# Optimization experiments

Hardware: AMD Instinct MI355X
Metric: run time of the kernel (lower is better)

Reference implementation:

```python
import jax, jax.numpy as jnp
import numpy as np

NEG_SLOPE_GAT = 0.2   # PyG GATConv default negative_slope
NEG_SLOPE = 0.01      # torch.nn.LeakyReLU default
NUM_AISLES = 20       # aisle_nrs drawn from [0,20); matches aisle_nrs.max()+1


def leaky(x, s):
    return jnp.where(x >= 0, x, s * x)


def gat_conv(x, src, dst, W, a_src, a_dst, b, n_nodes):
    """Single-head PyG GATConv (self-loops already appended to src/dst)."""
    h = x @ W                                        # [N, C]
    es = h @ a_src                                   # [N]
    ed = h @ a_dst                                   # [N]
    e = leaky(es[src] + ed[dst], NEG_SLOPE_GAT)      # [E] per-edge score
    m = jax.ops.segment_max(e, dst, num_segments=n_nodes)
    w = jnp.exp(e - m[dst])
    z = jax.ops.segment_sum(w, dst, num_segments=n_nodes)
    alpha = w / z[dst]                               # segment softmax over incoming edges
    out = jax.ops.segment_sum(h[src] * alpha[:, None], dst, num_segments=n_nodes)
    return out + b


def setup_inputs() -> dict:
    key = jax.random.key(0)
    ks = jax.random.split(key, 32)
    B, N, E = 16, 2048, 32768
    Fin, H, O, HA = 32, 128, 64, 256

    def glorot(k, shape):
        fan = shape[0] + shape[-1]
        return jax.random.uniform(k, shape, jnp.float32, -1.0, 1.0) * np.sqrt(6.0 / fan)

    inp = {
        "graph_nodes": jax.random.normal(ks[0], (B, N, Fin), jnp.float32),
        "aisle_nrs": jax.random.randint(ks[1], (B, N), 0, NUM_AISLES),
        "graph_edge_links": jax.random.randint(ks[2], (B, 2, E), 0, N),
        "mask": jax.random.randint(ks[3], (B, N), 0, 2),
        "picks_left": jax.random.randint(ks[4], (B,), 0, 100),
        # GAT layer 1: Fin -> H
        "W1": glorot(ks[5], (Fin, H)), "as1": glorot(ks[6], (H,)), "ad1": glorot(ks[7], (H,)), "b1": jnp.zeros((H,), jnp.float32),
        # GAT layer 2: H -> H
        "W2": glorot(ks[8], (H, H)), "as2": glorot(ks[9], (H,)), "ad2": glorot(ks[10], (H,)), "b2": jnp.zeros((H,), jnp.float32),
        # GAT layer 3: H -> O
        "W3": glorot(ks[11], (H, O)), "as3": glorot(ks[12], (O,)), "ad3": glorot(ks[13], (O,)), "b3": jnp.zeros((O,), jnp.float32),
        # post-embedding MLP head
        "lw1": glorot(ks[14], (2 * O, HA)), "lb1": jnp.zeros((HA,), jnp.float32),
        "lw2": glorot(ks[15], (HA, O)), "lb2": jnp.zeros((O,), jnp.float32),
        "lw3": glorot(ks[16], (O, 1)), "lb3": jnp.zeros((1,), jnp.float32),
    }
    return inp


def reference(graph_nodes, aisle_nrs, graph_edge_links, mask, picks_left,
              W1, as1, ad1, b1, W2, as2, ad2, b2, W3, as3, ad3, b3,
              lw1, lb1, lw2, lb2, lw3, lb3):
    B, N, Fin = graph_nodes.shape
    NT = B * N
    x = graph_nodes.reshape(NT, Fin)

    # batch the graphs: offset per-graph edge indices, append self-loops
    off = (jnp.arange(B) * N)[:, None]
    src = (graph_edge_links[:, 0, :] + off).reshape(-1)
    dst = (graph_edge_links[:, 1, :] + off).reshape(-1)
    loops = jnp.arange(NT)
    src = jnp.concatenate([src, loops])
    dst = jnp.concatenate([dst, loops])

    x = gat_conv(x, src, dst, W1, as1, ad1, b1, NT)
    x = gat_conv(x, src, dst, W2, as2, ad2, b2, NT)
    x = gat_conv(x, src, dst, W3, as3, ad3, b3, NT)

    # scatter-mean aisle embedding
    batch_idx = jnp.repeat(jnp.arange(B), N)
    aid = aisle_nrs.reshape(-1) + batch_idx * NUM_AISLES   # [NT]
    S = B * NUM_AISLES
    ssum = jax.ops.segment_sum(x, aid, num_segments=S)
    cnt = jax.ops.segment_sum(jnp.ones((NT,), x.dtype), aid, num_segments=S)
    emb = ssum / jnp.maximum(cnt, 1.0)[:, None]

    x = jnp.concatenate([x, emb[aid]], axis=1)             # [NT, 2*O]
    x = leaky(x @ lw1 + lb1, NEG_SLOPE)
    x = leaky(x @ lw2 + lb2, NEG_SLOPE)
    x = (x @ lw3 + lb3).reshape(B, N)

    logits = jnp.where(mask != 0, x, -jnp.inf)
    return jax.nn.softmax(logits, axis=1)
```

## Files before the change

kernel.cpp:

```cpp
#include <hip/hip_runtime.h>
#include <hip/hip_bf16.h>
#include <math.h>

#define BATCH 16
#define NNODE 2048
#define EPG   32768
#define NT    (BATCH * NNODE)
#define ET    (BATCH * EPG + NT)
#define NUM_AISLES 20
#define SEG   (BATCH * NUM_AISLES)
#define NEG_GAT 0.2f
#define NEG_MLP 0.01f
#define ACHUNK 8
#define CAP 64

typedef __attribute__((ext_vector_type(8))) short s16x8;
typedef __attribute__((ext_vector_type(4))) float f32x4;

__device__ __forceinline__ void split_bf16(float v, unsigned short& hi, unsigned short& lo) {
    unsigned int u = __float_as_uint(v);
    unsigned int r = u + 0x7FFFu + ((u >> 16) & 1u);
    hi = (unsigned short)(r >> 16);
    float fh = __uint_as_float(((unsigned int)hi) << 16);
    float rem = v - fh;
    unsigned int u2 = __float_as_uint(rem);
    unsigned int r2 = u2 + 0x7FFFu + ((u2 >> 16) & 1u);
    lo = (unsigned short)(r2 >> 16);
}

#define WT_W1  0
#define WT_W2  4096
#define WT_W3  20480
#define WT_LW1 28672
#define WT_LW2 61440
#define WT_TOT 77824

__global__ __launch_bounds__(256) void wsplit_kernel(const float* __restrict__ W1,
                                                     const float* __restrict__ W2,
                                                     const float* __restrict__ W3,
                                                     const float* __restrict__ lw1,
                                                     const float* __restrict__ lw2,
                                                     unsigned short* __restrict__ wt_hi,
                                                     unsigned short* __restrict__ wt_lo) {
    int idx = blockIdx.x * 256 + threadIdx.x;
    if (idx >= WT_TOT) return;
    const float* src;
    int base, K, N;
    if (idx < WT_W2)      { src = W1;  base = WT_W1;  K = 32;  N = 128; }
    else if (idx < WT_W3) { src = W2;  base = WT_W2;  K = 128; N = 128; }
    else if (idx < WT_LW1){ src = W3;  base = WT_W3;  K = 128; N = 64;  }
    else if (idx < WT_LW2){ src = lw1; base = WT_LW1; K = 128; N = 256; }
    else                  { src = lw2; base = WT_LW2; K = 256; N = 64;  }
    int local = idx - base;
    int k = local / N;
    int n = local - k * N;
    unsigned short hi, lo;
    split_bf16(src[(size_t)k * N + n], hi, lo);
    wt_hi[base + (size_t)n * K + k] = hi;
    wt_lo[base + (size_t)n * K + k] = lo;
}

__global__ __launch_bounds__(256) void edge_scatter(const int* __restrict__ links,
                                                    int* __restrict__ cnt,
                                                    int* __restrict__ col_bkt) {
    int b = blockIdx.x;
    int s, d;
    if (b < 2048) {
        int xcd = b & 7, idx = b >> 3;
        int g = xcd * 2 + (idx >> 7);
        int chunk = idx & 127;
        int i = chunk * 256 + threadIdx.x;
        const int* pb = links + (size_t)g * 2 * EPG;
        s = pb[i] + (g << 11);
        d = pb[EPG + i] + (g << 11);
    } else {
        int b2 = b - 2048;
        int xcd = b2 & 7, idx = b2 >> 3;
        int g = xcd * 2 + (idx >> 3);
        int chunk = idx & 7;
        s = d = g * NNODE + chunk * 256 + threadIdx.x;
    }
    int pos = atomicAdd(&cnt[d], 1);
    if (pos < CAP) col_bkt[d * CAP + pos] = s;
}

template <int K, int NOUT, int COLS, bool LEAKY, bool ATTN, bool FINAL, bool CONCAT>
__global__ __launch_bounds__(256) void gemm_mfma(const float* __restrict__ A,
                                                 const unsigned short* __restrict__ wt_hi,
                                                 const unsigned short* __restrict__ wt_lo,
                                                 const float* __restrict__ bias,
                                                 float* __restrict__ out,
                                                 const float* __restrict__ a_src,
                                                 const float* __restrict__ a_dst,
                                                 float* __restrict__ es,
                                                 float* __restrict__ ed,
                                                 const float* __restrict__ emb,
                                                 const int* __restrict__ aisle,
                                                 const float* __restrict__ lw3,
                                                 const float* __restrict__ lb3,
                                                 const int* __restrict__ mask,
                                                 float* __restrict__ logits) {
    constexpr int C = COLS / 16;

    const int tid = threadIdx.x;
    const int wave = tid >> 6, lane = tid & 63;
    const int quad = lane >> 4, l15 = lane & 15;
    const int row0 = blockIdx.x * 64;
    const int c0 = blockIdx.y * COLS;
    const int m = row0 + wave * 16 + l15;

    f32x4 acc[C];
#pragma unroll
    for (int c = 0; c < C; ++c)
#pragma unroll
        for (int v = 0; v < 4; ++v) acc[c][v] = 0.f;

    union SU { s16x8 v; unsigned short u[8]; };

    for (int kc = 0; kc < K; kc += 32) {
        const int off = kc + quad * 8;
        const float* srcp;
        if constexpr (CONCAT) {
            if (off < 64) {
                srcp = A + (size_t)m * 64 + off;
            } else {
                int g = m >> 11;
                srcp = emb + ((size_t)(g * NUM_AISLES + aisle[m])) * 64 + (off - 64);
            }
        } else {
            srcp = A + (size_t)m * K + off;
        }
        float4 v0 = ((const float4*)srcp)[0];
        float4 v1 = ((const float4*)srcp)[1];
        float a8[8] = {v0.x, v0.y, v0.z, v0.w, v1.x, v1.y, v1.z, v1.w};
        SU ah, al;
#pragma unroll
        for (int j = 0; j < 8; ++j) split_bf16(a8[j], ah.u[j], al.u[j]);

#pragma unroll
        for (int c = 0; c < C; ++c) {
            size_t woff = (size_t)(c0 + c * 16 + l15) * K + kc + quad * 8;
            s16x8 wh = *(const s16x8*)(wt_hi + woff);
            s16x8 wl = *(const s16x8*)(wt_lo + woff);
            acc[c] = __builtin_amdgcn_mfma_f32_16x16x32_bf16(ah.v, wh, acc[c], 0, 0, 0);
            acc[c] = __builtin_amdgcn_mfma_f32_16x16x32_bf16(ah.v, wl, acc[c], 0, 0, 0);
            acc[c] = __builtin_amdgcn_mfma_f32_16x16x32_bf16(al.v, wh, acc[c], 0, 0, 0);
        }
    }
    if constexpr (FINAL) {
#pragma unroll
        for (int reg = 0; reg < 4; ++reg) {
            float p = 0.f;
#pragma unroll
            for (int c = 0; c < C; ++c) {
                int colx = c * 16 + l15;
                float v = acc[c][reg] + bias[colx];
                v = v >= 0.f ? v : NEG_MLP * v;
                p += v * lw3[colx];
            }
#pragma unroll
            for (int mk = 1; mk < 16; mk <<= 1) p += __shfl_xor(p, mk, 64);
            if (l15 == 0) {
                int row = row0 + wave * 16 + quad * 4 + reg;
                float lg = p + lb3[0];
                logits[row] = (mask[row] != 0) ? lg : -INFINITY;
            }
        }
    } else {
#pragma unroll
        for (int c = 0; c < C; ++c) {
            int colx = c0 + c * 16 + l15;
            float bv = bias ? bias[colx] : 0.f;
#pragma unroll
            for (int reg = 0; reg < 4; ++reg) {
                int row = row0 + wave * 16 + quad * 4 + reg;
                float v = acc[c][reg] + bv;
                if (LEAKY) v = v >= 0.f ? v : NEG_MLP * v;
                out[(size_t)row * NOUT + colx] = v;
            }
        }
        if constexpr (ATTN) {
#pragma unroll
            for (int reg = 0; reg < 4; ++reg) {
                float ps = 0.f, pd = 0.f;
#pragma unroll
                for (int c = 0; c < C; ++c) {
                    int colx = c * 16 + l15;
                    float v = acc[c][reg];
                    ps += v * a_src[colx];
                    pd += v * a_dst[colx];
                }
#pragma unroll
                for (int mk = 1; mk < 16; mk <<= 1) {
                    ps += __shfl_xor(ps, mk, 64);
                    pd += __shfl_xor(pd, mk, 64);
                }
                if (l15 == 0) {
                    int row = row0 + wave * 16 + quad * 4 + reg;
                    es[row] = ps;
                    ed[row] = pd;
                }
            }
        }
    }
}

template <int HD>
__global__ __launch_bounds__(256) void gat_aggregate(const float* __restrict__ h,
                                                     const float* __restrict__ es,
                                                     const float* __restrict__ ed,
                                                     const int* __restrict__ cnt,
                                                     const int* __restrict__ col_bkt,
                                                     const float* __restrict__ bias,
                                                     float* __restrict__ out) {
    int b = blockIdx.x;
    int xcd = b & 7, q = b >> 3;
    int graph = xcd * 2 + (q >> 9);
    int node = graph * NNODE + (q & 511) * 4 + (threadIdx.x >> 6);
    int lane = threadIdx.x & 63;
    int deg = cnt[node];
    deg = deg < CAP ? deg : CAP;
    float edv = ed[node];

    float e0 = -INFINITY;
    int c0v = 0;
    if (lane < deg) {
        c0v = col_bkt[node * CAP + lane];
        float e = es[c0v] + edv;
        e0 = e >= 0.f ? e : NEG_GAT * e;
    }
    float m = e0;
#pragma unroll
    for (int off = 32; off; off >>= 1) m = fmaxf(m, __shfl_xor(m, off, 64));
    float z = __expf(e0 - m);
#pragma unroll
    for (int off = 32; off; off >>= 1) z += __shfl_xor(z, off, 64);
    float w0 = __expf(e0 - m) / z;

    const int quad = lane >> 4, l15 = lane & 15;
    if (HD == 128) {
        float a0 = 0.f, a1 = 0.f, a2 = 0.f, a3 = 0.f;
        float a4 = 0.f, a5 = 0.f, a6 = 0.f, a7 = 0.f;
        for (int jj = 0; jj < deg; jj += 4) {
            int j2 = jj + quad;
            int s = __shfl(c0v, j2, 64);
            float w = __shfl(w0, j2, 64);
            const float* base = h + (size_t)s * 128 + l15 * 8;
            float4 v0 = *(const float4*)base;
            float4 v1 = *(const float4*)(base + 4);
            a0 += w * v0.x; a1 += w * v0.y; a2 += w * v0.z; a3 += w * v0.w;
            a4 += w * v1.x; a5 += w * v1.y; a6 += w * v1.z; a7 += w * v1.w;
        }
#pragma unroll
        for (int off = 16; off <= 32; off <<= 1) {
            a0 += __shfl_xor(a0, off, 64); a1 += __shfl_xor(a1, off, 64);
            a2 += __shfl_xor(a2, off, 64); a3 += __shfl_xor(a3, off, 64);
            a4 += __shfl_xor(a4, off, 64); a5 += __shfl_xor(a5, off, 64);
            a6 += __shfl_xor(a6, off, 64); a7 += __shfl_xor(a7, off, 64);
        }
        if (quad == 0) {
            const float* bb = bias + l15 * 8;
            float4 o0, o1;
            o0.x = a0 + bb[0]; o0.y = a1 + bb[1]; o0.z = a2 + bb[2]; o0.w = a3 + bb[3];
            o1.x = a4 + bb[4]; o1.y = a5 + bb[5]; o1.z = a6 + bb[6]; o1.w = a7 + bb[7];
            float* op = out + (size_t)node * 128 + l15 * 8;
            *(float4*)op = o0;
            *(float4*)(op + 4) = o1;
        }
    } else {
        float a0 = 0.f, a1 = 0.f, a2 = 0.f, a3 = 0.f;
        for (int jj = 0; jj < deg; jj += 4) {
            int j2 = jj + quad;
            int s = __shfl(c0v, j2, 64);
            float w = __shfl(w0, j2, 64);
            float4 v = *(const float4*)(h + (size_t)s * 64 + l15 * 4);
            a0 += w * v.x; a1 += w * v.y; a2 += w * v.z; a3 += w * v.w;
        }
#pragma unroll
        for (int off = 16; off <= 32; off <<= 1) {
            a0 += __shfl_xor(a0, off, 64); a1 += __shfl_xor(a1, off, 64);
            a2 += __shfl_xor(a2, off, 64); a3 += __shfl_xor(a3, off, 64);
        }
        if (quad == 0) {
            const float* bb = bias + l15 * 4;
            float4 o;
            o.x = a0 + bb[0]; o.y = a1 + bb[1]; o.z = a2 + bb[2]; o.w = a3 + bb[3];
            *(float4*)(out + (size_t)node * 64 + l15 * 4) = o;
        }
    }
}

__global__ __launch_bounds__(256) void aisle_partial(const float* __restrict__ x3,
                                                     const int* __restrict__ aisle,
                                                     float* __restrict__ psum,
                                                     int* __restrict__ pcnt) {
    int g = blockIdx.x >> 3;
    int ch = blockIdx.x & 7;
    int f = threadIdx.x & 63;
    int stripe = threadIdx.x >> 6;

    __shared__ float sacc[4][NUM_AISLES][64];
    __shared__ int scnt[4][NUM_AISLES];
    for (int i = threadIdx.x; i < 4 * NUM_AISLES * 64; i += 256)
        ((float*)sacc)[i] = 0.f;
    for (int i = threadIdx.x; i < 4 * NUM_AISLES; i += 256)
        ((int*)scnt)[i] = 0;
    __syncthreads();

    const int* ai = aisle + g * NNODE;
    const float* xg = x3 + (size_t)g * NNODE * 64;
    int n0 = ch * 256 + stripe * 64;
#pragma unroll 4
    for (int i = 0; i < 64; ++i) {
        int n = n0 + i;
        int a = ai[n];
        float v = xg[(size_t)n * 64 + f];
        sacc[stripe][a][f] += v;
        if (f == 0) scnt[stripe][a]++;
    }
    __syncthreads();

    for (int i = threadIdx.x; i < NUM_AISLES * 64; i += 256) {
        int a = i >> 6, ff = i & 63;
        psum[((size_t)blockIdx.x * NUM_AISLES + a) * 64 + ff] =
            sacc[0][a][ff] + sacc[1][a][ff] + sacc[2][a][ff] + sacc[3][a][ff];
    }
    for (int i = threadIdx.x; i < NUM_AISLES; i += 256) {
        pcnt[blockIdx.x * NUM_AISLES + i] =
            scnt[0][i] + scnt[1][i] + scnt[2][i] + scnt[3][i];
    }
}

__global__ __launch_bounds__(256) void aisle_reduce(const float* __restrict__ psum,
                                                    const int* __restrict__ pcnt,
                                                    float* __restrict__ emb) {
    int idx = blockIdx.x * 256 + threadIdx.x;
    if (idx >= SEG * 64) return;
    int seg = idx >> 6;
    int f = idx & 63;
    int g = seg / NUM_AISLES;
    int a = seg - g * NUM_AISLES;
    float s = 0.f;
    int c = 0;
#pragma unroll
    for (int ch = 0; ch < ACHUNK; ++ch) {
        int blk = g * ACHUNK + ch;
        s += psum[((size_t)blk * NUM_AISLES + a) * 64 + f];
        c += pcnt[blk * NUM_AISLES + a];
    }
    emb[idx] = s / fmaxf((float)c, 1.0f);
}

__global__ __launch_bounds__(256) void softmax_kernel(const float* __restrict__ logits,
                                                      float* __restrict__ out) {
    int b = blockIdx.x;
    const float* lr = logits + b * NNODE;
    __shared__ float red[4], redz[4];
    float m = -INFINITY;
    for (int i = threadIdx.x; i < NNODE; i += 256) m = fmaxf(m, lr[i]);
#pragma unroll
    for (int off = 32; off; off >>= 1) m = fmaxf(m, __shfl_xor(m, off, 64));
    if ((threadIdx.x & 63) == 0) red[threadIdx.x >> 6] = m;
    __syncthreads();
    m = fmaxf(fmaxf(red[0], red[1]), fmaxf(red[2], red[3]));
    float z = 0.f;
    for (int i = threadIdx.x; i < NNODE; i += 256) z += __expf(lr[i] - m);
#pragma unroll
    for (int off = 32; off; off >>= 1) z += __shfl_xor(z, off, 64);
    if ((threadIdx.x & 63) == 0) redz[threadIdx.x >> 6] = z;
    __syncthreads();
    z = redz[0] + redz[1] + redz[2] + redz[3];
    float invz = 1.0f / z;
    for (int i = threadIdx.x; i < NNODE; i += 256) {
        float v = lr[i];
        out[b * NNODE + i] = (v == -INFINITY) ? 0.f : __expf(v - m) * invz;
    }
}


extern "C" void kernel_launch(void* const* d_in, const int* in_sizes, int n_in,
                              void* d_out, int out_size, void* d_ws, size_t ws_size,
                              hipStream_t stream) {
    const float* gn   = (const float*)d_in[0];
    const int* aisle  = (const int*)d_in[1];
    const int* links  = (const int*)d_in[2];
    const int* mask   = (const int*)d_in[3];
    const float* W1  = (const float*)d_in[5];
    const float* as1 = (const float*)d_in[6];
    const float* ad1 = (const float*)d_in[7];
    const float* b1  = (const float*)d_in[8];
    const float* W2  = (const float*)d_in[9];
    const float* as2 = (const float*)d_in[10];
    const float* ad2 = (const float*)d_in[11];
    const float* b2  = (const float*)d_in[12];
    const float* W3  = (const float*)d_in[13];
    const float* as3 = (const float*)d_in[14];
    const float* ad3 = (const float*)d_in[15];
    const float* b3  = (const float*)d_in[16];
    const float* lw1 = (const float*)d_in[17];
    const float* lb1 = (const float*)d_in[18];
    const float* lw2 = (const float*)d_in[19];
    const float* lb2 = (const float*)d_in[20];
    const float* lw3 = (const float*)d_in[21];
    const float* lb3 = (const float*)d_in[22];
    float* out = (float*)d_out;

    float* ws = (float*)d_ws;
    float* h      = ws;
    float* xb     = h + (size_t)NT * 128;
    float* es     = xb + (size_t)NT * 128;
    float* ed     = es + NT;
    float* emb    = ed + NT;
    float* y1     = emb + SEG * 64;
    float* y2     = y1 + (size_t)NT * 256;
    float* logits = y2 + (size_t)NT * 64;
    float* psum   = logits + NT;
    int* pcnt     = (int*)(psum + 128 * NUM_AISLES * 64);
    int* row_ptr  = pcnt + 128 * NUM_AISLES;
    int* cnt      = row_ptr + NT + 1;
    int* col_bkt  = (int*)y2;
    unsigned short* wt_hi = (unsigned short*)(((uintptr_t)(cnt + NT) + 63) & ~(uintptr_t)63);
    unsigned short* wt_lo = wt_hi + ((WT_TOT + 31) & ~31);

    const int EB = (ET + 255) / 256;

    wsplit_kernel<<<(WT_TOT + 255) / 256, 256, 0, stream>>>(W1, W2, W3, lw1, lw2, wt_hi, wt_lo);
    hipMemsetAsync(cnt, 0, NT * sizeof(int), stream);
    edge_scatter<<<EB, 256, 0, stream>>>(links, cnt, col_bkt);

    gemm_mfma<32, 128, 128, false, true, false, false><<<dim3(NT / 64, 1), 256, 0, stream>>>(
        gn, wt_hi + WT_W1, wt_lo + WT_W1, nullptr, h, as1, ad1, es, ed,
        nullptr, nullptr, nullptr, nullptr, nullptr, nullptr);
    gat_aggregate<128><<<NT / 4, 256, 0, stream>>>(h, es, ed, cnt, col_bkt, b1, xb);

    gemm_mfma<128, 128, 128, false, true, false, false><<<dim3(NT / 64, 1), 256, 0, stream>>>(
        xb, wt_hi + WT_W2, wt_lo + WT_W2, nullptr, h, as2, ad2, es, ed,
        nullptr, nullptr, nullptr, nullptr, nullptr, nullptr);
    gat_aggregate<128><<<NT / 4, 256, 0, stream>>>(h, es, ed, cnt, col_bkt, b2, xb);

    gemm_mfma<128, 64, 64, false, true, false, false><<<dim3(NT / 64, 1), 256, 0, stream>>>(
        xb, wt_hi + WT_W3, wt_lo + WT_W3, nullptr, h, as3, ad3, es, ed,
        nullptr, nullptr, nullptr, nullptr, nullptr, nullptr);
    gat_aggregate<64><<<NT / 4, 256, 0, stream>>>(h, es, ed, cnt, col_bkt, b3, xb);

    aisle_partial<<<BATCH * ACHUNK, 256, 0, stream>>>(xb, aisle, psum, pcnt);
    aisle_reduce<<<(SEG * 64 + 255) / 256, 256, 0, stream>>>(psum, pcnt, emb);

    gemm_mfma<128, 256, 128, true, false, false, true><<<dim3(NT / 64, 2), 256, 0, stream>>>(
        xb, wt_hi + WT_LW1, wt_lo + WT_LW1, lb1, y1, nullptr, nullptr, nullptr, nullptr,
        emb, aisle, nullptr, nullptr, nullptr, nullptr);
    gemm_mfma<256, 64, 64, true, false, true, false><<<dim3(NT / 64, 1), 256, 0, stream>>>(
        y1, wt_hi + WT_LW2, wt_lo + WT_LW2, lb2, y2, nullptr, nullptr, nullptr, nullptr,
        nullptr, nullptr, lw3, lb3, mask, logits);

    softmax_kernel<<<BATCH, 256, 0, stream>>>(logits, out);
}
```

Baseline: 340.7 us.

## Split weights into bf16 hi/lo inside GEMM and stage them in LDS

```diff
diff --git a/kernel.cpp b/kernel.cpp
--- a/kernel.cpp
+++ b/kernel.cpp
@@ -26,38 +26,6 @@
     unsigned int u2 = __float_as_uint(rem);
     unsigned int r2 = u2 + 0x7FFFu + ((u2 >> 16) & 1u);
     lo = (unsigned short)(r2 >> 16);
-}
-
-#define WT_W1  0
-#define WT_W2  4096
-#define WT_W3  20480
-#define WT_LW1 28672
-#define WT_LW2 61440
-#define WT_TOT 77824
-
-__global__ __launch_bounds__(256) void wsplit_kernel(const float* __restrict__ W1,
-                                                     const float* __restrict__ W2,
-                                                     const float* __restrict__ W3,
-                                                     const float* __restrict__ lw1,
-                                                     const float* __restrict__ lw2,
-                                                     unsigned short* __restrict__ wt_hi,
-                                                     unsigned short* __restrict__ wt_lo) {
-    int idx = blockIdx.x * 256 + threadIdx.x;
-    if (idx >= WT_TOT) return;
-    const float* src;
-    int base, K, N;
-    if (idx < WT_W2)      { src = W1;  base = WT_W1;  K = 32;  N = 128; }
-    else if (idx < WT_W3) { src = W2;  base = WT_W2;  K = 128; N = 128; }
-    else if (idx < WT_LW1){ src = W3;  base = WT_W3;  K = 128; N = 64;  }
-    else if (idx < WT_LW2){ src = lw1; base = WT_LW1; K = 128; N = 256; }
-    else                  { src = lw2; base = WT_LW2; K = 256; N = 64;  }
-    int local = idx - base;
-    int k = local / N;
-    int n = local - k * N;
-    unsigned short hi, lo;
-    split_bf16(src[(size_t)k * N + n], hi, lo);
-    wt_hi[base + (size_t)n * K + k] = hi;
-    wt_lo[base + (size_t)n * K + k] = lo;
 }
 
 __global__ __launch_bounds__(256) void edge_scatter(const int* __restrict__ links,
@@ -86,8 +54,7 @@
 
 template <int K, int NOUT, int COLS, bool LEAKY, bool ATTN, bool FINAL, bool CONCAT>
 __global__ __launch_bounds__(256) void gemm_mfma(const float* __restrict__ A,
-                                                 const unsigned short* __restrict__ wt_hi,
-                                                 const unsigned short* __restrict__ wt_lo,
+                                                 const float* __restrict__ W,
                                                  const float* __restrict__ bias,
                                                  float* __restrict__ out,
                                                  const float* __restrict__ a_src,
@@ -101,6 +68,9 @@
                                                  const int* __restrict__ mask,
                                                  float* __restrict__ logits) {
     constexpr int C = COLS / 16;
+    constexpr int LDW = K + 8;
+
+    __shared__ unsigned short Wh[COLS * LDW], Wl[COLS * LDW];
 
     const int tid = threadIdx.x;
     const int wave = tid >> 6, lane = tid & 63;
@@ -108,6 +78,16 @@
     const int row0 = blockIdx.x * 64;
     const int c0 = blockIdx.y * COLS;
     const int m = row0 + wave * 16 + l15;
+
+    for (int i = tid; i < K * COLS; i += 256) {
+        int k = i / COLS;
+        int n = i - k * COLS;
+        unsigned short h, l;
+        split_bf16(W[(size_t)k * NOUT + c0 + n], h, l);
+        Wh[n * LDW + k] = h;
+        Wl[n * LDW + k] = l;
+    }
+    __syncthreads();
 
     f32x4 acc[C];
 #pragma unroll
@@ -139,9 +119,9 @@
 
 #pragma unroll
         for (int c = 0; c < C; ++c) {
-            size_t woff = (size_t)(c0 + c * 16 + l15) * K + kc + quad * 8;
-            s16x8 wh = *(const s16x8*)(wt_hi + woff);
-            s16x8 wl = *(const s16x8*)(wt_lo + woff);
+            int woff = (c * 16 + l15) * LDW + kc + quad * 8;
+            s16x8 wh = *(const s16x8*)&Wh[woff];
+            s16x8 wl = *(const s16x8*)&Wl[woff];
             acc[c] = __builtin_amdgcn_mfma_f32_16x16x32_bf16(ah.v, wh, acc[c], 0, 0, 0);
             acc[c] = __builtin_amdgcn_mfma_f32_16x16x32_bf16(ah.v, wl, acc[c], 0, 0, 0);
             acc[c] = __builtin_amdgcn_mfma_f32_16x16x32_bf16(al.v, wh, acc[c], 0, 0, 0);
@@ -419,39 +399,31 @@
     int* row_ptr  = pcnt + 128 * NUM_AISLES;
     int* cnt      = row_ptr + NT + 1;
     int* col_bkt  = (int*)y2;
-    unsigned short* wt_hi = (unsigned short*)(((uintptr_t)(cnt + NT) + 63) & ~(uintptr_t)63);
-    unsigned short* wt_lo = wt_hi + ((WT_TOT + 31) & ~31);
 
     const int EB = (ET + 255) / 256;
 
-    wsplit_kernel<<<(WT_TOT + 255) / 256, 256, 0, stream>>>(W1, W2, W3, lw1, lw2, wt_hi, wt_lo);
     hipMemsetAsync(cnt, 0, NT * sizeof(int), stream);
     edge_scatter<<<EB, 256, 0, stream>>>(links, cnt, col_bkt);
 
     gemm_mfma<32, 128, 128, false, true, false, false><<<dim3(NT / 64, 1), 256, 0, stream>>>(
-        gn, wt_hi + WT_W1, wt_lo + WT_W1, nullptr, h, as1, ad1, es, ed,
-        nullptr, nullptr, nullptr, nullptr, nullptr, nullptr);
+        gn, W1, nullptr, h, as1, ad1, es, ed, nullptr, nullptr, nullptr, nullptr, nullptr, nullptr);
     gat_aggregate<128><<<NT / 4, 256, 0, stream>>>(h, es, ed, cnt, col_bkt, b1, xb);
 
     gemm_mfma<128, 128, 128, false, true, false, false><<<dim3(NT / 64, 1), 256, 0, stream>>>(
-        xb, wt_hi + WT_W2, wt_lo + WT_W2, nullptr, h, as2, ad2, es, ed,
-        nullptr, nullptr, nullptr, nullptr, nullptr, nullptr);
+        xb, W2, nullptr, h, as2, ad2, es, ed, nullptr, nullptr, nullptr, nullptr, nullptr, nullptr);
     gat_aggregate<128><<<NT / 4, 256, 0, stream>>>(h, es, ed, cnt, col_bkt, b2, xb);
 
     gemm_mfma<128, 64, 64, false, true, false, false><<<dim3(NT / 64, 1), 256, 0, stream>>>(
-        xb, wt_hi + WT_W3, wt_lo + WT_W3, nullptr, h, as3, ad3, es, ed,
-        nullptr, nullptr, nullptr, nullptr, nullptr, nullptr);
+        xb, W3, nullptr, h, as3, ad3, es, ed, nullptr, nullptr, nullptr, nullptr, nullptr, nullptr);
     gat_aggregate<64><<<NT / 4, 256, 0, stream>>>(h, es, ed, cnt, col_bkt, b3, xb);
 
     aisle_partial<<<BATCH * ACHUNK, 256, 0, stream>>>(xb, aisle, psum, pcnt);
     aisle_reduce<<<(SEG * 64 + 255) / 256, 256, 0, stream>>>(psum, pcnt, emb);
 
     gemm_mfma<128, 256, 128, true, false, false, true><<<dim3(NT / 64, 2), 256, 0, stream>>>(
-        xb, wt_hi + WT_LW1, wt_lo + WT_LW1, lb1, y1, nullptr, nullptr, nullptr, nullptr,
-        emb, aisle, nullptr, nullptr, nullptr, nullptr);
+        xb, lw1, lb1, y1, nullptr, nullptr, nullptr, nullptr, emb, aisle, nullptr, nullptr, nullptr, nullptr);
     gemm_mfma<256, 64, 64, true, false, true, false><<<dim3(NT / 64, 1), 256, 0, stream>>>(
-        y1, wt_hi + WT_LW2, wt_lo + WT_LW2, lb2, y2, nullptr, nullptr, nullptr, nullptr,
-        nullptr, nullptr, lw3, lb3, mask, logits);
+        y1, lw2, lb2, y2, nullptr, nullptr, nullptr, nullptr, nullptr, nullptr, lw3, lb3, mask, logits);
 
     softmax_kernel<<<BATCH, 256, 0, stream>>>(logits, out);
 }
```

Measured after the change: 313.3 us. -8.0%, faster.
